# Kernel optimization log

Hardware: AMD Instinct MI355X
Metric: run time of the kernel (lower is better)

Reference implementation:

```python
import jax, jax.numpy as jnp
import numpy as np

P = 12            # synapses per neuron (hardcoded in module)
WRES = 3
WMAX = 2 ** WRES - 1  # 7
THETA = 30
Q = 524288


def setup_inputs() -> dict:
    key = jax.random.key(0)
    k1, k2 = jax.random.split(key)
    data = jax.random.uniform(k1, (2, 2), dtype=jnp.float32)
    # w_init='uniform': randint in [0, wmax] cast to float
    weights = jax.random.randint(k2, (Q, P), 0, WMAX + 1).astype(jnp.float32)
    return {"data": data, "weights": weights}


def reference(data, weights):
    q = weights.shape[0]
    # data.unfold(0,2,1).unfold(1,2,1) on a 2x2 input -> one (2,2) patch;
    patch_tiled = jnp.tile(data, (3, 1)).reshape(-1)           # (12,)
    inp = jnp.broadcast_to(patch_tiled, (q, P))                # (q, 12) input spiketimes

    # zero effective weight for Inf (null) inputs
    eff_w = jnp.where(jnp.isinf(inp), 0.0, weights)

    # sort spike times per neuron, gather weights in arrival order
    sorted_idx = jnp.argsort(inp, axis=1)
    sorted_times = jnp.take_along_axis(inp, sorted_idx, axis=1)
    sorted_w = jnp.take_along_axis(eff_w, sorted_idx, axis=1)

    # cumulative body potential; first index crossing theta fires
    cpot = jnp.cumsum(sorted_w, axis=1)                        # (q, 12)
    fired = (cpot >= THETA).astype(jnp.int32)
    dec = jnp.arange(P, 0, -1, dtype=jnp.int32)
    idx = jnp.argmax(fired * dec, axis=1)                      # first firing position
    rows = jnp.arange(q)
    ec = sorted_times[rows, idx]
    null = jnp.sum(fired, axis=1) == 0                         # never crossed theta
    ec = jnp.where(null, jnp.inf, ec)
    pot = cpot[rows, idx]

    # RNL refinement: scan wmax candidate output times, ramp-no-leak response.
    # Computed for all rows (identical math), applied only where not null
    # (torch version uses boolean indexing; masking is the jit-friendly form).
    rnl_t = ec[:, None] + jnp.arange(WMAX, dtype=jnp.float32)  # (q, wmax)
    resp = jnp.clip(
        jnp.minimum(rnl_t[:, :, None] + 1.0 - inp[:, None, :],
                    weights[:, None, :]),
        0.0)                                                   # (q, wmax, 12)
    respsum = jnp.sum(resp, axis=2)                            # (q, wmax)
    fired2 = (respsum >= THETA).astype(jnp.int32)
    dec2 = jnp.arange(WMAX, 0, -1, dtype=jnp.int32)
    idx2 = jnp.argmax(fired2 * dec2, axis=1)
    ec_rnl = ec + idx2.astype(jnp.float32)
    pot_rnl = respsum[rows, idx2]
    nonnull = ~null
    ec = jnp.where(nonnull, ec_rnl, ec)
    pot = jnp.where(nonnull, pot_rnl, pot)

    # winner-take-all over the q neurons of the single column:
    ec2 = ec.reshape(1, q)
    pot2 = pot.reshape(1, q)
    minv = jnp.min(ec2, axis=1)                                # (1,)
    modpot = jnp.where(ec2 == minv[:, None], pot2, -1.0)
    iid = jnp.argmax(modpot, axis=1)                           # (1,)
    li = jnp.full((1, q), jnp.inf, dtype=ec.dtype)
    li = li.at[jnp.arange(1), iid].set(minv)

    out_next = li.reshape(1, 1, q)                # output_spiketimes_nextlayer
    out_stdp = jnp.broadcast_to(li.reshape(-1)[:, None], (q, P))
    return out_next, inp, out_stdp
```

## Files before the change

### kernel.cpp

```cpp
#include <hip/hip_runtime.h>
#include <float.h>

#define QN 524288
#define NB1 1024


typedef unsigned int uint;
typedef unsigned short ushort;

__device__ __forceinline__ float bf2f(ushort b) {
    return __uint_as_float(((uint)b) << 16);
}
__device__ __forceinline__ ushort f2bf(float f) {
    uint u = __float_as_uint(f);
    uint r = (u + 0x7FFFu + ((u >> 16) & 1u)) >> 16;
    return (ushort)r;
}

__device__ __forceinline__ bool better(float ea, float pa, int ia,
                                       float eb, float pb, int ib) {
    if (ea < eb) return true;
    if (ea > eb) return false;
    if (pa > pb) return true;
    if (pa < pb) return false;
    return ia < ib;
}

__global__ __launch_bounds__(256) void tnn_compute(
    const ushort* __restrict__ data, const ushort* __restrict__ w,
    float* __restrict__ bec, float* __restrict__ bpot, int* __restrict__ bidx)
{
    __shared__ int sp[12];
    __shared__ float s_ec[256], s_pot[256];
    __shared__ int s_idx[256];

    float dv[4] = {bf2f(data[0]), bf2f(data[1]), bf2f(data[2]), bf2f(data[3])};

    if (threadIdx.x < 12) {
        int j = threadIdx.x;
        float tj = dv[j & 3];
        int rank = 0;
        #pragma unroll
        for (int k = 0; k < 12; ++k) {
            float tk = dv[k & 3];
            if (tk < tj || (tk == tj && k < j)) rank++;
        }
        sp[rank] = j;
    }
    __syncthreads();

    int perm[12];
    #pragma unroll
    for (int r = 0; r < 12; ++r) perm[r] = sp[r];

    float best_ec = INFINITY, best_pot = -INFINITY;
    int best_i = 0x7fffffff;

    for (int i = blockIdx.x * blockDim.x + threadIdx.x; i < QN;
         i += gridDim.x * blockDim.x) {
        const uint2* p = (const uint2*)(w + (size_t)i * 12);
        uint2 a = p[0], b = p[1], c = p[2];
        float wv[12];
        wv[0]  = bf2f((ushort)(a.x & 0xFFFF)); wv[1]  = bf2f((ushort)(a.x >> 16));
        wv[2]  = bf2f((ushort)(a.y & 0xFFFF)); wv[3]  = bf2f((ushort)(a.y >> 16));
        wv[4]  = bf2f((ushort)(b.x & 0xFFFF)); wv[5]  = bf2f((ushort)(b.x >> 16));
        wv[6]  = bf2f((ushort)(b.y & 0xFFFF)); wv[7]  = bf2f((ushort)(b.y >> 16));
        wv[8]  = bf2f((ushort)(c.x & 0xFFFF)); wv[9]  = bf2f((ushort)(c.x >> 16));
        wv[10] = bf2f((ushort)(c.y & 0xFFFF)); wv[11] = bf2f((ushort)(c.y >> 16));

        float cp = 0.0f, cp0 = 0.0f;
        int idx = -1;
        #pragma unroll
        for (int r = 0; r < 12; ++r) {
            cp += wv[perm[r]];
            if (r == 0) cp0 = cp;
            if (idx < 0 && cp >= 30.0f) idx = r;
        }

        float ec, pot;
        if (idx >= 0) {
            float ec0 = dv[perm[idx] & 3];
            float rs0 = 0.0f, chosen = 0.0f;
            int idx2 = -1;
            for (int cdt = 0; cdt < 7; ++cdt) {
                float v = (ec0 + (float)cdt) + 1.0f;
                float s = 0.0f;
                #pragma unroll
                for (int j = 0; j < 12; ++j) {
                    float r = v - dv[j & 3];
                    r = fminf(r, wv[j]);
                    r = fmaxf(r, 0.0f);
                    s += r;
                }
                if (cdt == 0) rs0 = s;
                if (s >= 30.0f) { idx2 = cdt; chosen = s; break; }
            }
            if (idx2 < 0) { idx2 = 0; chosen = rs0; }
            ec = ec0 + (float)idx2;
            pot = chosen;
        } else {
            ec = INFINITY;
            pot = cp0;
        }

        if (better(ec, pot, i, best_ec, best_pot, best_i)) {
            best_ec = ec; best_pot = pot; best_i = i;
        }
    }

    int tid = threadIdx.x;
    s_ec[tid] = best_ec; s_pot[tid] = best_pot; s_idx[tid] = best_i;
    __syncthreads();
    for (int off = 128; off > 0; off >>= 1) {
        if (tid < off) {
            if (better(s_ec[tid + off], s_pot[tid + off], s_idx[tid + off],
                       s_ec[tid], s_pot[tid], s_idx[tid])) {
                s_ec[tid] = s_ec[tid + off];
                s_pot[tid] = s_pot[tid + off];
                s_idx[tid] = s_idx[tid + off];
            }
        }
        __syncthreads();
    }
    if (tid == 0) {
        bec[blockIdx.x] = s_ec[0];
        bpot[blockIdx.x] = s_pot[0];
        bidx[blockIdx.x] = s_idx[0];
    }
}

__global__ __launch_bounds__(256) void tnn_wta(
    const float* __restrict__ bec, const float* __restrict__ bpot,
    const int* __restrict__ bidx, float* __restrict__ winner)
{
    __shared__ float s_ec[256], s_pot[256];
    __shared__ int s_idx[256];
    int tid = threadIdx.x;
    float e = INFINITY, p = -INFINITY;
    int ix = 0x7fffffff;
    for (int i = tid; i < NB1; i += 256) {
        float be = bec[i], bp = bpot[i];
        int bi = bidx[i];
        if (better(be, bp, bi, e, p, ix)) { e = be; p = bp; ix = bi; }
    }
    s_ec[tid] = e; s_pot[tid] = p; s_idx[tid] = ix;
    __syncthreads();
    for (int off = 128; off > 0; off >>= 1) {
        if (tid < off) {
            if (better(s_ec[tid + off], s_pot[tid + off], s_idx[tid + off],
                       s_ec[tid], s_pot[tid], s_idx[tid])) {
                s_ec[tid] = s_ec[tid + off];
                s_pot[tid] = s_pot[tid + off];
                s_idx[tid] = s_idx[tid + off];
            }
        }
        __syncthreads();
    }
    if (tid == 0) {
        winner[0] = s_ec[0];
        ((int*)winner)[1] = s_idx[0];
    }
}

__global__ __launch_bounds__(256) void tnn_write(
    const ushort* __restrict__ data, const float* __restrict__ winner,
    uint4* __restrict__ out)
{
    float minv = winner[0];
    int iid = ((const int*)winner)[1];
    ushort mbf = f2bf(minv);
    if ((ushort)(mbf & 0x7FFF) >= (ushort)0x7F80) mbf = 0x7F7F;
    const ushort BIGF = 0x7F7F;

    uint P01 = (uint)data[0] | ((uint)data[1] << 16);
    uint P23 = (uint)data[2] | ((uint)data[3] << 16);
    uint4 PAT  = make_uint4(P01, P23, P01, P23);
    uint BB = (uint)BIGF | ((uint)BIGF << 16);
    uint4 BIG4 = make_uint4(BB, BB, BB, BB);

    const int NEXT4 = QN / 8;
    const int ROW4  = (QN * 3) / 2;
    uint4* next4 = out;
    uint4* inp4  = out + NEXT4;
    uint4* stdp4 = out + NEXT4 + ROW4;

    int t = blockIdx.x * blockDim.x + threadIdx.x;
    if (t >= ROW4) return;

    inp4[t] = PAT;

    long e0  = (long)t * 8;
    long wlo = (long)iid * 12, whi = wlo + 12;
    if (e0 + 8 > wlo && e0 < whi) {
        ushort v[8];
        #pragma unroll
        for (int k = 0; k < 8; ++k) {
            long e = e0 + k;
            v[k] = (e >= wlo && e < whi) ? mbf : BIGF;
        }
        uint4 o;
        o.x = (uint)v[0] | ((uint)v[1] << 16); o.y = (uint)v[2] | ((uint)v[3] << 16);
        o.z = (uint)v[4] | ((uint)v[5] << 16); o.w = (uint)v[6] | ((uint)v[7] << 16);
        stdp4[t] = o;
    } else {
        stdp4[t] = BIG4;
    }

    if (t < NEXT4) {
        long n0 = (long)t * 8;
        if (iid >= n0 && iid < n0 + 8) {
            ushort v[8];
            #pragma unroll
            for (int k = 0; k < 8; ++k) v[k] = (n0 + k == iid) ? mbf : BIGF;
            uint4 o;
            o.x = (uint)v[0] | ((uint)v[1] << 16); o.y = (uint)v[2] | ((uint)v[3] << 16);
            o.z = (uint)v[4] | ((uint)v[5] << 16); o.w = (uint)v[6] | ((uint)v[7] << 16);
            next4[t] = o;
        } else {
            next4[t] = BIG4;
        }
    }
}

extern "C" void kernel_launch(void* const* d_in, const int* in_sizes, int n_in,
                              void* d_out, int out_size, void* d_ws, size_t ws_size,
                              hipStream_t stream) {
    const ushort* data = (const ushort*)d_in[0];
    const ushort* w    = (const ushort*)d_in[1];
    uint4* out = (uint4*)d_out;

    float* bec  = (float*)d_ws;
    float* bpot = bec + NB1;
    int*   bidx = (int*)(bpot + NB1);
    float* winner = (float*)(bidx + NB1);

    tnn_compute<<<NB1, 256, 0, stream>>>(data, w, bec, bpot, bidx);
    tnn_wta<<<1, 256, 0, stream>>>(bec, bpot, bidx, winner);
    tnn_write<<<(QN * 3) / 2 / 256, 256, 0, stream>>>(data, winner, out);
}
```

Measured before the change: 95.26 us.

## Fuse bulk output writes into compute kernel and patch winner in finalize

```diff
diff --git a/kernel.cpp b/kernel.cpp
--- a/kernel.cpp
+++ b/kernel.cpp
@@ -1,8 +1,8 @@
 #include <hip/hip_runtime.h>
 #include <float.h>
 
-#define QN 524288
-#define NB1 1024
+#define QN   524288
+#define NBLK 2048
 
 
 typedef unsigned int uint;
@@ -13,8 +13,7 @@
 }
 __device__ __forceinline__ ushort f2bf(float f) {
     uint u = __float_as_uint(f);
-    uint r = (u + 0x7FFFu + ((u >> 16) & 1u)) >> 16;
-    return (ushort)r;
+    return (ushort)((u + 0x7FFFu + ((u >> 16) & 1u)) >> 16);
 }
 
 __device__ __forceinline__ bool better(float ea, float pa, int ia,
@@ -26,15 +25,40 @@
     return ia < ib;
 }
 
-__global__ __launch_bounds__(256) void tnn_compute(
+__global__ __launch_bounds__(256) void tnn_fused(
     const ushort* __restrict__ data, const ushort* __restrict__ w,
+    uint4* __restrict__ out,
     float* __restrict__ bec, float* __restrict__ bpot, int* __restrict__ bidx)
 {
     __shared__ int sp[12];
     __shared__ float s_ec[256], s_pot[256];
     __shared__ int s_idx[256];
 
+    const int T = NBLK * 256;
+    const int t = blockIdx.x * 256 + threadIdx.x;
+
     float dv[4] = {bf2f(data[0]), bf2f(data[1]), bf2f(data[2]), bf2f(data[3])};
+    uint P01 = (uint)data[0] | ((uint)data[1] << 16);
+    uint P23 = (uint)data[2] | ((uint)data[3] << 16);
+    uint4 PAT  = make_uint4(P01, P23, P01, P23);
+    uint BB = 0x7F7F7F7Fu & 0xFFFFFFFFu;
+    BB = (uint)0x7F7F | ((uint)0x7F7F << 16);
+    uint4 BIG4 = make_uint4(BB, BB, BB, BB);
+
+    const int NEXT4 = QN / 8;
+    const int ROW4  = (QN * 3) / 2;
+    uint4* next4 = out;
+    uint4* inp4  = out + NEXT4;
+    uint4* stdp4 = out + NEXT4 + ROW4;
+
+    const uint2* p = (const uint2*)(w + (size_t)t * 12);
+    uint2 a = p[0], b = p[1], c = p[2];
+
+    inp4[t]  = PAT;
+    stdp4[t] = BIG4;
+    int t2 = t + T;
+    if (t2 < ROW4) { inp4[t2] = PAT; stdp4[t2] = BIG4; }
+    if (t < NEXT4) next4[t] = BIG4;
 
     if (threadIdx.x < 12) {
         int j = threadIdx.x;
@@ -48,68 +72,55 @@
         sp[rank] = j;
     }
     __syncthreads();
-
     int perm[12];
     #pragma unroll
     for (int r = 0; r < 12; ++r) perm[r] = sp[r];
 
-    float best_ec = INFINITY, best_pot = -INFINITY;
-    int best_i = 0x7fffffff;
+    float wv[12];
+    wv[0]  = bf2f((ushort)(a.x & 0xFFFF)); wv[1]  = bf2f((ushort)(a.x >> 16));
+    wv[2]  = bf2f((ushort)(a.y & 0xFFFF)); wv[3]  = bf2f((ushort)(a.y >> 16));
+    wv[4]  = bf2f((ushort)(b.x & 0xFFFF)); wv[5]  = bf2f((ushort)(b.x >> 16));
+    wv[6]  = bf2f((ushort)(b.y & 0xFFFF)); wv[7]  = bf2f((ushort)(b.y >> 16));
+    wv[8]  = bf2f((ushort)(c.x & 0xFFFF)); wv[9]  = bf2f((ushort)(c.x >> 16));
+    wv[10] = bf2f((ushort)(c.y & 0xFFFF)); wv[11] = bf2f((ushort)(c.y >> 16));
 
-    for (int i = blockIdx.x * blockDim.x + threadIdx.x; i < QN;
-         i += gridDim.x * blockDim.x) {
-        const uint2* p = (const uint2*)(w + (size_t)i * 12);
-        uint2 a = p[0], b = p[1], c = p[2];
-        float wv[12];
-        wv[0]  = bf2f((ushort)(a.x & 0xFFFF)); wv[1]  = bf2f((ushort)(a.x >> 16));
-        wv[2]  = bf2f((ushort)(a.y & 0xFFFF)); wv[3]  = bf2f((ushort)(a.y >> 16));
-        wv[4]  = bf2f((ushort)(b.x & 0xFFFF)); wv[5]  = bf2f((ushort)(b.x >> 16));
-        wv[6]  = bf2f((ushort)(b.y & 0xFFFF)); wv[7]  = bf2f((ushort)(b.y >> 16));
-        wv[8]  = bf2f((ushort)(c.x & 0xFFFF)); wv[9]  = bf2f((ushort)(c.x >> 16));
-        wv[10] = bf2f((ushort)(c.y & 0xFFFF)); wv[11] = bf2f((ushort)(c.y >> 16));
+    float cp = 0.0f, cp0 = 0.0f;
+    int idx = -1;
+    #pragma unroll
+    for (int r = 0; r < 12; ++r) {
+        cp += wv[perm[r]];
+        if (r == 0) cp0 = cp;
+        if (idx < 0 && cp >= 30.0f) idx = r;
+    }
 
-        float cp = 0.0f, cp0 = 0.0f;
-        int idx = -1;
-        #pragma unroll
-        for (int r = 0; r < 12; ++r) {
-            cp += wv[perm[r]];
-            if (r == 0) cp0 = cp;
-            if (idx < 0 && cp >= 30.0f) idx = r;
+    float ec, pot;
+    if (idx >= 0) {
+        float ec0 = dv[perm[idx] & 3];
+        float rs0 = 0.0f, chosen = 0.0f;
+        int idx2 = -1;
+        for (int cdt = 0; cdt < 7; ++cdt) {
+            float v = (ec0 + (float)cdt) + 1.0f;
+            float s = 0.0f;
+            #pragma unroll
+            for (int j = 0; j < 12; ++j) {
+                float r = v - dv[j & 3];
+                r = fminf(r, wv[j]);
+                r = fmaxf(r, 0.0f);
+                s += r;
+            }
+            if (cdt == 0) rs0 = s;
+            if (s >= 30.0f) { idx2 = cdt; chosen = s; break; }
         }
-
-        float ec, pot;
-        if (idx >= 0) {
-            float ec0 = dv[perm[idx] & 3];
-            float rs0 = 0.0f, chosen = 0.0f;
-            int idx2 = -1;
-            for (int cdt = 0; cdt < 7; ++cdt) {
-                float v = (ec0 + (float)cdt) + 1.0f;
-                float s = 0.0f;
-                #pragma unroll
-                for (int j = 0; j < 12; ++j) {
-                    float r = v - dv[j & 3];
-                    r = fminf(r, wv[j]);
-                    r = fmaxf(r, 0.0f);
-                    s += r;
-                }
-                if (cdt == 0) rs0 = s;
-                if (s >= 30.0f) { idx2 = cdt; chosen = s; break; }
-            }
-            if (idx2 < 0) { idx2 = 0; chosen = rs0; }
-            ec = ec0 + (float)idx2;
-            pot = chosen;
-        } else {
-            ec = INFINITY;
-            pot = cp0;
-        }
-
-        if (better(ec, pot, i, best_ec, best_pot, best_i)) {
-            best_ec = ec; best_pot = pot; best_i = i;
-        }
+        if (idx2 < 0) { idx2 = 0; chosen = rs0; }
+        ec = ec0 + (float)idx2;
+        pot = chosen;
+    } else {
+        ec = INFINITY;
+        pot = cp0;
     }
 
     int tid = threadIdx.x;
-    s_ec[tid] = best_ec; s_pot[tid] = best_pot; s_idx[tid] = best_i;
+    s_ec[tid] = ec; s_pot[tid] = pot; s_idx[tid] = t;
     __syncthreads();
     for (int off = 128; off > 0; off >>= 1) {
         if (tid < off) {
@@ -129,16 +140,16 @@
     }
 }
 
-__global__ __launch_bounds__(256) void tnn_wta(
+__global__ __launch_bounds__(256) void tnn_finalize(
     const float* __restrict__ bec, const float* __restrict__ bpot,
-    const int* __restrict__ bidx, float* __restrict__ winner)
+    const int* __restrict__ bidx, ushort* __restrict__ out)
 {
     __shared__ float s_ec[256], s_pot[256];
     __shared__ int s_idx[256];
     int tid = threadIdx.x;
     float e = INFINITY, p = -INFINITY;
     int ix = 0x7fffffff;
-    for (int i = tid; i < NB1; i += 256) {
+    for (int i = tid; i < NBLK; i += 256) {
         float be = bec[i], bp = bpot[i];
         int bi = bidx[i];
         if (better(be, bp, bi, e, p, ix)) { e = be; p = bp; ix = bi; }
@@ -156,69 +167,17 @@
         }
         __syncthreads();
     }
-    if (tid == 0) {
-        winner[0] = s_ec[0];
-        ((int*)winner)[1] = s_idx[0];
-    }
-}
-
-__global__ __launch_bounds__(256) void tnn_write(
-    const ushort* __restrict__ data, const float* __restrict__ winner,
-    uint4* __restrict__ out)
-{
-    float minv = winner[0];
-    int iid = ((const int*)winner)[1];
-    ushort mbf = f2bf(minv);
-    if ((ushort)(mbf & 0x7FFF) >= (ushort)0x7F80) mbf = 0x7F7F;
-    const ushort BIGF = 0x7F7F;
-
-    uint P01 = (uint)data[0] | ((uint)data[1] << 16);
-    uint P23 = (uint)data[2] | ((uint)data[3] << 16);
-    uint4 PAT  = make_uint4(P01, P23, P01, P23);
-    uint BB = (uint)BIGF | ((uint)BIGF << 16);
-    uint4 BIG4 = make_uint4(BB, BB, BB, BB);
-
-    const int NEXT4 = QN / 8;
-    const int ROW4  = (QN * 3) / 2;
-    uint4* next4 = out;
-    uint4* inp4  = out + NEXT4;
-    uint4* stdp4 = out + NEXT4 + ROW4;
-
-    int t = blockIdx.x * blockDim.x + threadIdx.x;
-    if (t >= ROW4) return;
-
-    inp4[t] = PAT;
-
-    long e0  = (long)t * 8;
-    long wlo = (long)iid * 12, whi = wlo + 12;
-    if (e0 + 8 > wlo && e0 < whi) {
-        ushort v[8];
-        #pragma unroll
-        for (int k = 0; k < 8; ++k) {
-            long e = e0 + k;
-            v[k] = (e >= wlo && e < whi) ? mbf : BIGF;
+    if (tid < 13) {
+        float minv = s_ec[0];
+        int iid = s_idx[0];
+        ushort mbf;
+        if (isinf(minv)) mbf = 0x7F7F;
+        else {
+            mbf = f2bf(minv);
+            if ((ushort)(mbf & 0x7FFF) >= (ushort)0x7F80) mbf = 0x7F7F;
         }
-        uint4 o;
-        o.x = (uint)v[0] | ((uint)v[1] << 16); o.y = (uint)v[2] | ((uint)v[3] << 16);
-        o.z = (uint)v[4] | ((uint)v[5] << 16); o.w = (uint)v[6] | ((uint)v[7] << 16);
-        stdp4[t] = o;
-    } else {
-        stdp4[t] = BIG4;
-    }
-
-    if (t < NEXT4) {
-        long n0 = (long)t * 8;
-        if (iid >= n0 && iid < n0 + 8) {
-            ushort v[8];
-            #pragma unroll
-            for (int k = 0; k < 8; ++k) v[k] = (n0 + k == iid) ? mbf : BIGF;
-            uint4 o;
-            o.x = (uint)v[0] | ((uint)v[1] << 16); o.y = (uint)v[2] | ((uint)v[3] << 16);
-            o.z = (uint)v[4] | ((uint)v[5] << 16); o.w = (uint)v[6] | ((uint)v[7] << 16);
-            next4[t] = o;
-        } else {
-            next4[t] = BIG4;
-        }
+        if (tid == 0) out[iid] = mbf;
+        if (tid < 12) out[(size_t)13 * QN + (size_t)iid * 12 + tid] = mbf;
     }
 }
 
@@ -230,11 +189,9 @@
     uint4* out = (uint4*)d_out;
 
     float* bec  = (float*)d_ws;
-    float* bpot = bec + NB1;
-    int*   bidx = (int*)(bpot + NB1);
-    float* winner = (float*)(bidx + NB1);
+    float* bpot = bec + NBLK;
+    int*   bidx = (int*)(bpot + NBLK);
 
-    tnn_compute<<<NB1, 256, 0, stream>>>(data, w, bec, bpot, bidx);
-    tnn_wta<<<1, 256, 0, stream>>>(bec, bpot, bidx, winner);
-    tnn_write<<<(QN * 3) / 2 / 256, 256, 0, stream>>>(data, winner, out);
+    tnn_fused<<<NBLK, 256, 0, stream>>>(data, w, out, bec, bpot, bidx);
+    tnn_finalize<<<1, 256, 0, stream>>>(bec, bpot, bidx, (ushort*)d_out);
 }
```

Result: faster. 91.60 us (-3.8%).
